# Kernel optimization log

Hardware: AMD Instinct MI355X
Metric: run time of the kernel (lower is better)

## Reference

```python
import jax, jax.numpy as jnp
import numpy as np

DIM = 2048
HEADS = 16
HEAD_DIM = DIM // HEADS


def setup_inputs() -> dict:
    key = jax.random.key(0)
    ks = jax.random.split(key, 9)
    B, S = 1, 4096
    X = jax.random.normal(ks[0], (B, S, DIM), dtype=jnp.float32)
    sc = 1.0 / np.sqrt(DIM)
    Wq = jax.random.normal(ks[1], (DIM, DIM), dtype=jnp.float32) * sc
    bq = jax.random.normal(ks[2], (DIM,), dtype=jnp.float32) * 0.01
    Wk = jax.random.normal(ks[3], (DIM, DIM), dtype=jnp.float32) * sc
    bk = jax.random.normal(ks[4], (DIM,), dtype=jnp.float32) * 0.01
    Wv = jax.random.normal(ks[5], (DIM, DIM), dtype=jnp.float32) * sc
    bv = jax.random.normal(ks[6], (DIM,), dtype=jnp.float32) * 0.01
    Wo = jax.random.normal(ks[7], (DIM, DIM), dtype=jnp.float32) * sc
    bo = jax.random.normal(ks[8], (DIM,), dtype=jnp.float32) * 0.01
    return {"X": X, "Wq": Wq, "bq": bq, "Wk": Wk, "bk": bk,
            "Wv": Wv, "bv": bv, "Wo": Wo, "bo": bo, "is_causal": 1}


def reference(X, Wq, bq, Wk, bk, Wv, bv, Wo, bo, is_causal):
    B, S, _ = X.shape
    # torch nn.Linear: y = x @ W^T + b
    Q = (X @ Wq.T + bq).reshape(B, S, HEADS, HEAD_DIM).transpose(0, 2, 1, 3)
    K = (X @ Wk.T + bk).reshape(B, S, HEADS, HEAD_DIM).transpose(0, 2, 1, 3)
    V = (X @ Wv.T + bv).reshape(B, S, HEADS, HEAD_DIM).transpose(0, 2, 1, 3)
    scores = jnp.einsum('bhqd,bhkd->bhqk', Q, K) / np.sqrt(HEAD_DIM)  # [B,H,S,S]
    if is_causal:
        causal = jnp.tril(jnp.ones((S, S), dtype=bool))
        scores = jnp.where(causal, scores, -jnp.inf)
    attn = jax.nn.softmax(scores, axis=-1)
    # dropout_rate = 0 (eval) -> identity
    Out = jnp.einsum('bhqk,bhkd->bhqd', attn, V)
    Out = Out.transpose(0, 2, 1, 3).reshape(B, S, DIM)
    return Out @ Wo.T + bo
```

## Files before the change

### kernel.cpp

```cpp
#include <hip/hip_runtime.h>
#include <hip/hip_bf16.h>

typedef unsigned short u16;
typedef __attribute__((ext_vector_type(8))) short short8;
typedef __attribute__((ext_vector_type(4))) short short4v;
typedef __attribute__((ext_vector_type(4))) float floatx4;

constexpr int SEQ = 4096;
constexpr int DM  = 2048;
constexpr int NH  = 16;
constexpr int HD  = 128;

__device__ inline u16 f2b(float f) {
    __hip_bfloat16 h = __float2bfloat16(f);
    return *reinterpret_cast<u16*>(&h);
}
__device__ inline float b2f(u16 u) {
    __hip_bfloat16 h = *reinterpret_cast<__hip_bfloat16*>(&u);
    return __bfloat162float(h);
}

__device__ __forceinline__ void async_copy16(const u16* g, u16* lds_base) {
    __builtin_amdgcn_global_load_lds(
        (const __attribute__((address_space(1))) unsigned int*)g,
        (__attribute__((address_space(3))) unsigned int*)lds_base,
        16, 0, 0);
}

__global__ void detect_dtype(const u16* __restrict__ X, int* __restrict__ flag) {
    __shared__ int cnt;
    if (threadIdx.x == 0) cnt = 0;
    __syncthreads();
    int local = 0;
    for (int i = threadIdx.x; i < 4096; i += 256) {
        int e = (X[i] >> 7) & 0xFF;
        if (e >= 0x3C && e <= 0x8D) local++;
    }
    atomicAdd(&cnt, local);
    __syncthreads();
    if (threadIdx.x == 0) *flag = (cnt >= 3890) ? 1 : 0;
}

struct ConvArgs {
    const void* src[9];
    unsigned long long dstoff[9];
    int n[9];
};
__global__ void convert_all(ConvArgs a, u16* __restrict__ base,
                            const int* __restrict__ flag) {
    const int t = blockIdx.y;
    const int n = a.n[t];
    const int i = (blockIdx.x * blockDim.x + threadIdx.x) * 8;
    if (i >= n) return;
    u16* out = base + a.dstoff[t];
    if (*flag) {
        *(short8*)&out[i] = *(const short8*)&((const u16*)a.src[t])[i];
    } else {
        const float* p = (const float*)a.src[t];
        u16 tmp[8];
#pragma unroll
        for (int j = 0; j < 8; j++) tmp[j] = f2b(p[i + j]);
        *(short8*)&out[i] = *(const short8*)tmp;
    }
}

__device__ __forceinline__ void gemm256_core(
    const u16* __restrict__ A, const u16* __restrict__ W,
    int m0, int n0, floatx4 (&acc)[8][4])
{
    __shared__ __align__(16) u16 As[2][16384];
    __shared__ __align__(16) u16 Bs[2][16384];
    constexpr int K  = DM;
    constexpr int NT = K / 64;

    const int tid  = threadIdx.x;
    const int lane = tid & 63;
    const int w    = tid >> 6;
    const int qm   = lane & 15;
    const int quad = lane >> 4;
    const int wm   = (w >> 2) * 128;
    const int wn   = (w & 3) * 64;

    const int srow = tid >> 3;
    const int scol = ((tid & 7) ^ (srow & 7)) * 8;

    const int fo0 = (quad ^ (qm & 7)) * 8;
    const int fo1 = fo0 ^ 32;

    const u16* Ag = A + (size_t)(m0 + srow) * K + scol;
    const u16* Wg = W + (size_t)(n0 + srow) * K + scol;

#define STG_A4(par, k0) {                                                 \
    async_copy16(Ag + (size_t)0 * 64 * K + (k0), &As[par][0 * 4096 + w * 512]); \
    async_copy16(Ag + (size_t)1 * 64 * K + (k0), &As[par][1 * 4096 + w * 512]); \
    async_copy16(Ag + (size_t)2 * 64 * K + (k0), &As[par][2 * 4096 + w * 512]); \
    async_copy16(Ag + (size_t)3 * 64 * K + (k0), &As[par][3 * 4096 + w * 512]); }
#define STG_B4(par, k0) {                                                 \
    async_copy16(Wg + (size_t)0 * 64 * K + (k0), &Bs[par][0 * 4096 + w * 512]); \
    async_copy16(Wg + (size_t)1 * 64 * K + (k0), &Bs[par][1 * 4096 + w * 512]); \
    async_copy16(Wg + (size_t)2 * 64 * K + (k0), &Bs[par][2 * 4096 + w * 512]); \
    async_copy16(Wg + (size_t)3 * 64 * K + (k0), &Bs[par][3 * 4096 + w * 512]); }

#define RD_A(d0, d1, row) { d0 = *(const short8*)&Ac[(row) * 64 + fo0];   \
                            d1 = *(const short8*)&Ac[(row) * 64 + fo1]; }

#define MFMA_Q(q2, x00, x01, x10, x11) {                                  \
    __builtin_amdgcn_s_setprio(1);                                        \
    _Pragma("unroll")                                                     \
    for (int nt = 0; nt < 4; ++nt) {                                      \
        acc[q2][nt]     = __builtin_amdgcn_mfma_f32_16x16x32_bf16(x00, bf[nt][0], acc[q2][nt], 0, 0, 0);     \
        acc[q2][nt]     = __builtin_amdgcn_mfma_f32_16x16x32_bf16(x01, bf[nt][1], acc[q2][nt], 0, 0, 0);     \
        acc[q2 + 1][nt] = __builtin_amdgcn_mfma_f32_16x16x32_bf16(x10, bf[nt][0], acc[q2 + 1][nt], 0, 0, 0); \
        acc[q2 + 1][nt] = __builtin_amdgcn_mfma_f32_16x16x32_bf16(x11, bf[nt][1], acc[q2 + 1][nt], 0, 0, 0); \
    }                                                                     \
    __builtin_amdgcn_s_setprio(0); }

#pragma unroll
    for (int i = 0; i < 8; ++i)
#pragma unroll
        for (int j = 0; j < 4; ++j) acc[i][j] = floatx4{0.f, 0.f, 0.f, 0.f};

    STG_A4(0, 0);
    STG_B4(0, 0);
    STG_A4(1, 64);
    STG_B4(1, 64);
    asm volatile("s_waitcnt vmcnt(8)" ::: "memory");
    __builtin_amdgcn_s_barrier();
    asm volatile("" ::: "memory");

    for (int t = 0; t < NT; ++t) {
        const int p = t & 1;
        const u16* Ac = As[p];
        const u16* Bc = Bs[p];
        const bool more = (t + 2 < NT);
        const int kf = (t + 2) * 64;

        short8 bf[4][2];
        short8 a0, a1, a2, a3, b0, b1, b2, b3;
        short8 c0, c1, c2, c3, d0, d1, d2, d3;

#pragma unroll
        for (int nt = 0; nt < 4; ++nt) {
            const int br = wn + nt * 16 + qm;
            bf[nt][0] = *(const short8*)&Bc[br * 64 + fo0];
            bf[nt][1] = *(const short8*)&Bc[br * 64 + fo1];
        }
        RD_A(a0, a1, wm + qm);
        RD_A(a2, a3, wm + 16 + qm);
        RD_A(b0, b1, wm + 32 + qm);
        RD_A(b2, b3, wm + 48 + qm);
        MFMA_Q(0, a0, a1, a2, a3);

        RD_A(c0, c1, wm + 64 + qm);
        RD_A(c2, c3, wm + 80 + qm);
        MFMA_Q(2, b0, b1, b2, b3);

        asm volatile("" ::: "memory");
        __builtin_amdgcn_s_barrier();
        asm volatile("" ::: "memory");
        if (more) { STG_B4(p, kf); }

        RD_A(d0, d1, wm + 96 + qm);
        RD_A(d2, d3, wm + 112 + qm);
        MFMA_Q(4, c0, c1, c2, c3);

        MFMA_Q(6, d0, d1, d2, d3);

        if (more) asm volatile("s_waitcnt vmcnt(4)" ::: "memory");
        else      asm volatile("s_waitcnt vmcnt(0)" ::: "memory");
        __builtin_amdgcn_s_barrier();
        asm volatile("" ::: "memory");
        if (more) { STG_A4(p, kf); }
    }
#undef STG_A4
#undef STG_B4
#undef RD_A
#undef MFMA_Q
}

__launch_bounds__(512, 2)
__global__ void gemm_qkv(const u16* __restrict__ A, const u16* __restrict__ W,
                         const u16* __restrict__ bias,
                         u16* __restrict__ Qb, u16* __restrict__ Kb,
                         u16* __restrict__ VtG) {
    const int m0 = blockIdx.y * 256;
    const int n0 = blockIdx.x * 256;
    floatx4 acc[8][4];
    gemm256_core(A, W, m0, n0, acc);

    const int tid  = threadIdx.x;
    const int lane = tid & 63;
    const int w    = tid >> 6;
    const int qm   = lane & 15;
    const int quad = lane >> 4;
    const int wm   = (w >> 2) * 128;
    const int wn   = (w & 3) * 64;

    const int buf = n0 >> 11;
    if (buf < 2) {
        u16* Y = (buf == 0) ? Qb : Kb;
#pragma unroll
        for (int nt = 0; nt < 4; ++nt) {
            const int gcol = n0 + wn + nt * 16 + qm;
            const int col  = gcol & 2047;
            const float bv = b2f(bias[gcol]);
#pragma unroll
            for (int mt = 0; mt < 8; ++mt) {
                const int rbase = m0 + wm + mt * 16 + quad * 4;
#pragma unroll
                for (int r = 0; r < 4; ++r)
                    Y[(size_t)(rbase + r) * DM + col] = f2b(acc[mt][nt][r] + bv);
            }
        }
    } else {
#pragma unroll
        for (int nt = 0; nt < 4; ++nt) {
            const int gcol = n0 + wn + nt * 16 + qm;
            const int col  = gcol & 2047;
            const float bv = b2f(bias[gcol]);
#pragma unroll
            for (int mt = 0; mt < 8; ++mt) {
                const int rbase = m0 + wm + mt * 16 + quad * 4;
                u16 tmp[4];
#pragma unroll
                for (int r = 0; r < 4; ++r)
                    tmp[r] = f2b(acc[mt][nt][r] + bv);
                *(short4v*)&VtG[(size_t)col * SEQ + rbase] = *(const short4v*)tmp;
            }
        }
    }
}

__launch_bounds__(512, 2)
__global__ void gemm_out(const u16* __restrict__ A, const u16* __restrict__ W,
                         const u16* __restrict__ bias, void* __restrict__ out,
                         const int* __restrict__ flag) {
    const int m0 = blockIdx.y * 256;
    const int n0 = blockIdx.x * 256;
    floatx4 acc[8][4];
    gemm256_core(A, W, m0, n0, acc);

    const int tid  = threadIdx.x;
    const int lane = tid & 63;
    const int w    = tid >> 6;
    const int qm   = lane & 15;
    const int quad = lane >> 4;
    const int wm   = (w >> 2) * 128;
    const int wn   = (w & 3) * 64;
    const int N    = DM;

    const int f = *flag;
#pragma unroll
    for (int nt = 0; nt < 4; ++nt) {
        const int col = n0 + wn + nt * 16 + qm;
        const float bv = b2f(bias[col]);
#pragma unroll
        for (int mt = 0; mt < 8; ++mt) {
            const int rbase = m0 + wm + mt * 16 + quad * 4;
#pragma unroll
            for (int r = 0; r < 4; ++r) {
                const float v = acc[mt][nt][r] + bv;
                if (f) ((u16*)out)[(size_t)(rbase + r) * N + col] = f2b(v);
                else   ((float*)out)[(size_t)(rbase + r) * N + col] = v;
            }
        }
    }
}

__launch_bounds__(512)
__global__ void attn_kernel(const u16* __restrict__ Q, const u16* __restrict__ K,
                            const u16* __restrict__ Vt, u16* __restrict__ O,
                            const int* __restrict__ is_causal_p) {
    __shared__ __align__(16) u16 Ks[64][136];
    __shared__ __align__(16) u16 Vts[128][72];
    __shared__ __align__(16) u16 Pb[8][16][72];

    const int tid  = threadIdx.x;
    const int lane = tid & 63;
    const int w    = tid >> 6;
    const int qm   = lane & 15;
    const int quad = lane >> 4;
    const int xt   = ((blockIdx.y >> 3) & 1) ? (gridDim.x - 1 - blockIdx.x)
                                             : blockIdx.x;
    const int q0   = xt * 128;
    const int h    = blockIdx.y;
    const int causal = *is_causal_p;
    const float scale = 0.08838834764831845f;
    const float SHIFT = 16.0f;

    short8 qf[4];
    {
        const u16* qptr = Q + (size_t)(q0 + w * 16 + qm) * DM + h * HD;
#pragma unroll
        for (int kc = 0; kc < 4; kc++)
            qf[kc] = *(const short8*)&qptr[kc * 32 + quad * 8];
    }

    floatx4 o[8];
#pragma unroll
    for (int dt = 0; dt < 8; dt++) o[dt] = floatx4{0.f, 0.f, 0.f, 0.f};
    float l_part[4] = {0.f, 0.f, 0.f, 0.f};

    const int jend = causal ? (q0 + 128) : SEQ;

    const int kr0 = tid >> 4;
    const int kc8 = (tid & 15) * 8;
    const int vd0 = tid >> 3;
    const int vc8 = (tid & 7) * 8;

    short8 kreg[2], vreg[2];
#pragma unroll
    for (int p = 0; p < 2; p++) {
        kreg[p] = *(const short8*)&K[(size_t)(kr0 + p * 32) * DM + h * HD + kc8];
        vreg[p] = *(const short8*)&Vt[(size_t)(h * HD + vd0 + p * 64) * SEQ + vc8];
    }

    for (int j0 = 0; j0 < jend; j0 += 64) {
#pragma unroll
        for (int p = 0; p < 2; p++) {
            *(short8*)&Ks[kr0 + p * 32][kc8] = kreg[p];
            *(short8*)&Vts[vd0 + p * 64][vc8] = vreg[p];
        }
        __syncthreads();

        const int jn = (j0 + 64 < jend) ? j0 + 64 : 0;
#pragma unroll
        for (int p = 0; p < 2; p++) {
            kreg[p] = *(const short8*)&K[(size_t)(jn + kr0 + p * 32) * DM + h * HD + kc8];
            vreg[p] = *(const short8*)&Vt[(size_t)(h * HD + vd0 + p * 64) * SEQ + jn + vc8];
        }

        floatx4 s[4];
#pragma unroll
        for (int nt = 0; nt < 4; nt++) s[nt] = floatx4{0.f, 0.f, 0.f, 0.f};
#pragma unroll
        for (int kc = 0; kc < 4; kc++)
#pragma unroll
            for (int nt = 0; nt < 4; nt++) {
                short8 b = *(const short8*)&Ks[nt * 16 + qm][kc * 32 + quad * 8];
                s[nt] = __builtin_amdgcn_mfma_f32_16x16x32_bf16(qf[kc], b, s[nt], 0, 0, 0);
            }

        const bool mask = causal && (j0 + 64 > q0 + w * 16);
#pragma unroll
        for (int r = 0; r < 4; r++) {
            const int qg = q0 + w * 16 + quad * 4 + r;
#pragma unroll
            for (int nt = 0; nt < 4; nt++) {
                float v = fmaf(s[nt][r], scale, -SHIFT);
                if (mask && (j0 + nt * 16 + qm > qg)) v = -1e30f;
                const float p = __expf(v);
                l_part[r] += p;
                Pb[w][quad * 4 + r][nt * 16 + qm] = f2b(p);
            }
        }
        asm volatile("s_waitcnt lgkmcnt(0)" ::: "memory");

#pragma unroll
        for (int kc = 0; kc < 2; kc++) {
            short8 pf = *(const short8*)&Pb[w][qm][kc * 32 + quad * 8];
#pragma unroll
            for (int dt = 0; dt < 8; dt++) {
                short8 b = *(const short8*)&Vts[dt * 16 + qm][kc * 32 + quad * 8];
                o[dt] = __builtin_amdgcn_mfma_f32_16x16x32_bf16(pf, b, o[dt], 0, 0, 0);
            }
        }
        __syncthreads();
    }

#pragma unroll
    for (int r = 0; r < 4; r++) {
        float l = l_part[r];
#pragma unroll
        for (int off = 8; off >= 1; off >>= 1)
            l += __shfl_xor(l, off, 64);
        const float inv = 1.0f / l;
        const int qg = q0 + w * 16 + quad * 4 + r;
#pragma unroll
        for (int dt = 0; dt < 8; dt++) {
            const int d = h * HD + dt * 16 + qm;
            O[(size_t)qg * DM + d] = f2b(o[dt][r] * inv);
        }
    }
}

extern "C" void kernel_launch(void* const* d_in, const int* in_sizes, int n_in,
                              void* d_out, int out_size, void* d_ws, size_t ws_size,
                              hipStream_t stream) {
    const int* isc = (const int*)d_in[9];

    int* flag = (int*)d_ws;
    u16* base = (u16*)((char*)d_ws + 256);

    const int NX = SEQ * DM;
    const int NW = DM * DM;
    const int NB = DM;

    unsigned long long off = 0;
    const unsigned long long oXc   = off; off += NX;
    const unsigned long long oWall = off; off += 3ull * NW;
    const unsigned long long oWo   = off; off += NW;
    const unsigned long long oBall = off; off += 3ull * NB;
    const unsigned long long oBo   = off; off += NB;
    const unsigned long long oQ    = off; off += NX;
    const unsigned long long oK    = off; off += NX;
    const unsigned long long oVt   = off; off += NX;
    const unsigned long long oA    = off; off += NX;

    detect_dtype<<<1, 256, 0, stream>>>((const u16*)d_in[0], flag);

    ConvArgs ca;
    const unsigned long long dsts[9] = {oXc, oWall, oBall, oWall + NW, oBall + NB,
                                        oWall + 2ull * NW, oBall + 2ull * NB, oWo, oBo};
    for (int i = 0; i < 9; i++) {
        ca.src[i] = d_in[i];
        ca.dstoff[i] = dsts[i];
        ca.n[i] = in_sizes[i];
    }
    convert_all<<<dim3(NX / 8 / 256, 9), 256, 0, stream>>>(ca, base, flag);

    gemm_qkv<<<dim3(3 * DM / 256, SEQ / 256), 512, 0, stream>>>(
        base + oXc, base + oWall, base + oBall,
        base + oQ, base + oK, base + oVt);

    attn_kernel<<<dim3(SEQ / 128, NH), 512, 0, stream>>>(
        base + oQ, base + oK, base + oVt, base + oA, isc);

    gemm_out<<<dim3(DM / 256, SEQ / 256), 512, 0, stream>>>(
        base + oA, base + oWo, base + oBo, d_out, flag);
}
```

Baseline: 479.7 us.

## Shrink GEMM tiles to 256x128 to raise block count

Replaces the 256x256 GEMM tile with a 256x128 tile in both the QKV and output projections. Each wave now covers 64x64 instead of 128x64, the B staging and wait counts are halved to match, and the grids double. The aim is to fill more of the CUs, since the output GEMM previously launched only 128 blocks, and to reduce register pressure. The cost is lower arithmetic intensity per block, with more A-tile reloads and less operand reuse per MFMA.

```diff
diff --git a/kernel.cpp b/kernel.cpp
--- a/kernel.cpp
+++ b/kernel.cpp
@@ -64,12 +64,12 @@
     }
 }
 
-__device__ __forceinline__ void gemm256_core(
+__device__ __forceinline__ void gemm256x128_core(
     const u16* __restrict__ A, const u16* __restrict__ W,
-    int m0, int n0, floatx4 (&acc)[8][4])
+    int m0, int n0, floatx4 (&acc)[4][4])
 {
     __shared__ __align__(16) u16 As[2][16384];
-    __shared__ __align__(16) u16 Bs[2][16384];
+    __shared__ __align__(16) u16 Bs[2][8192];
     constexpr int K  = DM;
     constexpr int NT = K / 64;
 
@@ -78,8 +78,8 @@
     const int w    = tid >> 6;
     const int qm   = lane & 15;
     const int quad = lane >> 4;
-    const int wm   = (w >> 2) * 128;
-    const int wn   = (w & 3) * 64;
+    const int wm   = (w >> 1) * 64;
+    const int wn   = (w & 1) * 64;
 
     const int srow = tid >> 3;
     const int scol = ((tid & 7) ^ (srow & 7)) * 8;
@@ -95,36 +95,32 @@
     async_copy16(Ag + (size_t)1 * 64 * K + (k0), &As[par][1 * 4096 + w * 512]); \
     async_copy16(Ag + (size_t)2 * 64 * K + (k0), &As[par][2 * 4096 + w * 512]); \
     async_copy16(Ag + (size_t)3 * 64 * K + (k0), &As[par][3 * 4096 + w * 512]); }
-#define STG_B4(par, k0) {                                                 \
+#define STG_B2(par, k0) {                                                 \
     async_copy16(Wg + (size_t)0 * 64 * K + (k0), &Bs[par][0 * 4096 + w * 512]); \
-    async_copy16(Wg + (size_t)1 * 64 * K + (k0), &Bs[par][1 * 4096 + w * 512]); \
-    async_copy16(Wg + (size_t)2 * 64 * K + (k0), &Bs[par][2 * 4096 + w * 512]); \
-    async_copy16(Wg + (size_t)3 * 64 * K + (k0), &Bs[par][3 * 4096 + w * 512]); }
+    async_copy16(Wg + (size_t)1 * 64 * K + (k0), &Bs[par][1 * 4096 + w * 512]); }
 
 #define RD_A(d0, d1, row) { d0 = *(const short8*)&Ac[(row) * 64 + fo0];   \
                             d1 = *(const short8*)&Ac[(row) * 64 + fo1]; }
 
-#define MFMA_Q(q2, x00, x01, x10, x11) {                                  \
+#define MFMA_G(g, x0, x1) {                                               \
     __builtin_amdgcn_s_setprio(1);                                        \
     _Pragma("unroll")                                                     \
     for (int nt = 0; nt < 4; ++nt) {                                      \
-        acc[q2][nt]     = __builtin_amdgcn_mfma_f32_16x16x32_bf16(x00, bf[nt][0], acc[q2][nt], 0, 0, 0);     \
-        acc[q2][nt]     = __builtin_amdgcn_mfma_f32_16x16x32_bf16(x01, bf[nt][1], acc[q2][nt], 0, 0, 0);     \
-        acc[q2 + 1][nt] = __builtin_amdgcn_mfma_f32_16x16x32_bf16(x10, bf[nt][0], acc[q2 + 1][nt], 0, 0, 0); \
-        acc[q2 + 1][nt] = __builtin_amdgcn_mfma_f32_16x16x32_bf16(x11, bf[nt][1], acc[q2 + 1][nt], 0, 0, 0); \
+        acc[g][nt] = __builtin_amdgcn_mfma_f32_16x16x32_bf16(x0, rB[nt][0], acc[g][nt], 0, 0, 0); \
+        acc[g][nt] = __builtin_amdgcn_mfma_f32_16x16x32_bf16(x1, rB[nt][1], acc[g][nt], 0, 0, 0); \
     }                                                                     \
     __builtin_amdgcn_s_setprio(0); }
 
 #pragma unroll
-    for (int i = 0; i < 8; ++i)
+    for (int i = 0; i < 4; ++i)
 #pragma unroll
         for (int j = 0; j < 4; ++j) acc[i][j] = floatx4{0.f, 0.f, 0.f, 0.f};
 
     STG_A4(0, 0);
-    STG_B4(0, 0);
+    STG_B2(0, 0);
     STG_A4(1, 64);
-    STG_B4(1, 64);
-    asm volatile("s_waitcnt vmcnt(8)" ::: "memory");
+    STG_B2(1, 64);
+    asm volatile("s_waitcnt vmcnt(6)" ::: "memory");
     __builtin_amdgcn_s_barrier();
     asm volatile("" ::: "memory");
 
@@ -135,47 +131,42 @@
         const bool more = (t + 2 < NT);
         const int kf = (t + 2) * 64;
 
-        short8 bf[4][2];
-        short8 a0, a1, a2, a3, b0, b1, b2, b3;
-        short8 c0, c1, c2, c3, d0, d1, d2, d3;
+        short8 rB[4][2];
+        short8 a0, a1, a2, a3, b0, b1, c0, c1;
 
 #pragma unroll
         for (int nt = 0; nt < 4; ++nt) {
             const int br = wn + nt * 16 + qm;
-            bf[nt][0] = *(const short8*)&Bc[br * 64 + fo0];
-            bf[nt][1] = *(const short8*)&Bc[br * 64 + fo1];
+            rB[nt][0] = *(const short8*)&Bc[br * 64 + fo0];
+            rB[nt][1] = *(const short8*)&Bc[br * 64 + fo1];
         }
         RD_A(a0, a1, wm + qm);
         RD_A(a2, a3, wm + 16 + qm);
+        MFMA_G(0, a0, a1);
+
         RD_A(b0, b1, wm + 32 + qm);
-        RD_A(b2, b3, wm + 48 + qm);
-        MFMA_Q(0, a0, a1, a2, a3);
-
-        RD_A(c0, c1, wm + 64 + qm);
-        RD_A(c2, c3, wm + 80 + qm);
-        MFMA_Q(2, b0, b1, b2, b3);
+        MFMA_G(1, a2, a3);
 
         asm volatile("" ::: "memory");
         __builtin_amdgcn_s_barrier();
         asm volatile("" ::: "memory");
-        if (more) { STG_B4(p, kf); }
-
-        RD_A(d0, d1, wm + 96 + qm);
-        RD_A(d2, d3, wm + 112 + qm);
-        MFMA_Q(4, c0, c1, c2, c3);
-
-        MFMA_Q(6, d0, d1, d2, d3);
-
-        if (more) asm volatile("s_waitcnt vmcnt(4)" ::: "memory");
+        if (more) { STG_B2(p, kf); }
+
+        RD_A(c0, c1, wm + 48 + qm);
+        MFMA_G(2, b0, b1);
+
+        MFMA_G(3, c0, c1);
+
+        if (more) asm volatile("s_waitcnt vmcnt(2)" ::: "memory");
         else      asm volatile("s_waitcnt vmcnt(0)" ::: "memory");
         __builtin_amdgcn_s_barrier();
         asm volatile("" ::: "memory");
         if (more) { STG_A4(p, kf); }
     }
 #undef STG_A4
-#undef STG_B4
+#undef STG_B2
 #undef RD_A
-#undef MFMA_Q
+#undef MFMA_G
 }
 
 __launch_bounds__(512, 2)
@@ -184,17 +175,17 @@
                          u16* __restrict__ Qb, u16* __restrict__ Kb,
                          u16* __restrict__ VtG) {
     const int m0 = blockIdx.y * 256;
-    const int n0 = blockIdx.x * 256;
-    floatx4 acc[8][4];
-    gemm256_core(A, W, m0, n0, acc);
+    const int n0 = blockIdx.x * 128;
+    floatx4 acc[4][4];
+    gemm256x128_core(A, W, m0, n0, acc);
 
     const int tid  = threadIdx.x;
     const int lane = tid & 63;
     const int w    = tid >> 6;
     const int qm   = lane & 15;
     const int quad = lane >> 4;
-    const int wm   = (w >> 2) * 128;
-    const int wn   = (w & 3) * 64;
+    const int wm   = (w >> 1) * 64;
+    const int wn   = (w & 1) * 64;
 
     const int buf = n0 >> 11;
     if (buf < 2) {
@@ -205,7 +196,7 @@
             const int col  = gcol & 2047;
             const float bv = b2f(bias[gcol]);
 #pragma unroll
-            for (int mt = 0; mt < 8; ++mt) {
+            for (int mt = 0; mt < 4; ++mt) {
                 const int rbase = m0 + wm + mt * 16 + quad * 4;
 #pragma unroll
                 for (int r = 0; r < 4; ++r)
@@ -219,7 +210,7 @@
             const int col  = gcol & 2047;
             const float bv = b2f(bias[gcol]);
 #pragma unroll
-            for (int mt = 0; mt < 8; ++mt) {
+            for (int mt = 0; mt < 4; ++mt) {
                 const int rbase = m0 + wm + mt * 16 + quad * 4;
                 u16 tmp[4];
 #pragma unroll
@@ -236,17 +227,17 @@
                          const u16* __restrict__ bias, void* __restrict__ out,
                          const int* __restrict__ flag) {
     const int m0 = blockIdx.y * 256;
-    const int n0 = blockIdx.x * 256;
-    floatx4 acc[8][4];
-    gemm256_core(A, W, m0, n0, acc);
+    const int n0 = blockIdx.x * 128;
+    floatx4 acc[4][4];
+    gemm256x128_core(A, W, m0, n0, acc);
 
     const int tid  = threadIdx.x;
     const int lane = tid & 63;
     const int w    = tid >> 6;
     const int qm   = lane & 15;
     const int quad = lane >> 4;
-    const int wm   = (w >> 2) * 128;
-    const int wn   = (w & 3) * 64;
+    const int wm   = (w >> 1) * 64;
+    const int wn   = (w & 1) * 64;
     const int N    = DM;
 
     const int f = *flag;
@@ -255,7 +246,7 @@
         const int col = n0 + wn + nt * 16 + qm;
         const float bv = b2f(bias[col]);
 #pragma unroll
-        for (int mt = 0; mt < 8; ++mt) {
+        for (int mt = 0; mt < 4; ++mt) {
             const int rbase = m0 + wm + mt * 16 + quad * 4;
 #pragma unroll
             for (int r = 0; r < 4; ++r) {
@@ -419,13 +410,13 @@
     }
     convert_all<<<dim3(NX / 8 / 256, 9), 256, 0, stream>>>(ca, base, flag);
 
-    gemm_qkv<<<dim3(3 * DM / 256, SEQ / 256), 512, 0, stream>>>(
+    gemm_qkv<<<dim3(3 * DM / 128, SEQ / 256), 512, 0, stream>>>(
         base + oXc, base + oWall, base + oBall,
         base + oQ, base + oK, base + oVt);
 
     attn_kernel<<<dim3(SEQ / 128, NH), 512, 0, stream>>>(
         base + oQ, base + oK, base + oVt, base + oA, isc);
 
-    gemm_out<<<dim3(DM / 256, SEQ / 256), 512, 0, stream>>>(
+    gemm_out<<<dim3(DM / 128, SEQ / 256), 512, 0, stream>>>(
         base + oA, base + oWo, base + oBo, d_out, flag);
 }
```

After: 462.5 us. 3.6% less time.

## Restructure GEMM main loop into 4-phase ping-pong schedule with register prefetch

Applied to the files above, without the earlier changes.

Rewrites the 256x256 GEMM core loop as a two-tile unrolled body split into four MFMA phases. Each phase interleaves LDS fragment reads, async global-to-LDS stages and barriers, and the next tile's B and first A fragments are prefetched into alternate register sets. The aim is to overlap LDS reads and global loads with MFMA work and to spread the staging across the tile. In exchange it adds more barriers per tile and raises register pressure, and the waitcnt/barrier ordering assumes NT is even.

```diff
diff --git a/kernel.cpp b/kernel.cpp
--- a/kernel.cpp
+++ b/kernel.cpp
@@ -90,92 +90,107 @@
     const u16* Ag = A + (size_t)(m0 + srow) * K + scol;
     const u16* Wg = W + (size_t)(n0 + srow) * K + scol;
 
-#define STG_A4(par, k0) {                                                 \
+#define STG_A_ALL(par, k0) {                                                    \
     async_copy16(Ag + (size_t)0 * 64 * K + (k0), &As[par][0 * 4096 + w * 512]); \
     async_copy16(Ag + (size_t)1 * 64 * K + (k0), &As[par][1 * 4096 + w * 512]); \
     async_copy16(Ag + (size_t)2 * 64 * K + (k0), &As[par][2 * 4096 + w * 512]); \
     async_copy16(Ag + (size_t)3 * 64 * K + (k0), &As[par][3 * 4096 + w * 512]); }
-#define STG_B4(par, k0) {                                                 \
-    async_copy16(Wg + (size_t)0 * 64 * K + (k0), &Bs[par][0 * 4096 + w * 512]); \
-    async_copy16(Wg + (size_t)1 * 64 * K + (k0), &Bs[par][1 * 4096 + w * 512]); \
-    async_copy16(Wg + (size_t)2 * 64 * K + (k0), &Bs[par][2 * 4096 + w * 512]); \
-    async_copy16(Wg + (size_t)3 * 64 * K + (k0), &Bs[par][3 * 4096 + w * 512]); }
-
-#define RD_A(d0, d1, row) { d0 = *(const short8*)&Ac[(row) * 64 + fo0];   \
-                            d1 = *(const short8*)&Ac[(row) * 64 + fo1]; }
-
-#define MFMA_Q(q2, x00, x01, x10, x11) {                                  \
-    __builtin_amdgcn_s_setprio(1);                                        \
-    _Pragma("unroll")                                                     \
-    for (int nt = 0; nt < 4; ++nt) {                                      \
-        acc[q2][nt]     = __builtin_amdgcn_mfma_f32_16x16x32_bf16(x00, bf[nt][0], acc[q2][nt], 0, 0, 0);     \
-        acc[q2][nt]     = __builtin_amdgcn_mfma_f32_16x16x32_bf16(x01, bf[nt][1], acc[q2][nt], 0, 0, 0);     \
-        acc[q2 + 1][nt] = __builtin_amdgcn_mfma_f32_16x16x32_bf16(x10, bf[nt][0], acc[q2 + 1][nt], 0, 0, 0); \
-        acc[q2 + 1][nt] = __builtin_amdgcn_mfma_f32_16x16x32_bf16(x11, bf[nt][1], acc[q2 + 1][nt], 0, 0, 0); \
-    }                                                                     \
+#define STG_B_H(h, par, k0) {                                                   \
+    async_copy16(Wg + (size_t)(2*(h)) * 64 * K + (k0),                          \
+                 &Bs[par][(2*(h)) * 4096 + w * 512]);                           \
+    async_copy16(Wg + (size_t)(2*(h)+1) * 64 * K + (k0),                        \
+                 &Bs[par][(2*(h)+1) * 4096 + w * 512]); }
+
+#define RD_AQ(dst, Abase, q) {                                                  \
+    dst[0][0] = *(const short8*)&Abase[(wm + (2*(q)) * 16 + qm) * 64 + fo0];    \
+    dst[0][1] = *(const short8*)&Abase[(wm + (2*(q)) * 16 + qm) * 64 + fo1];    \
+    dst[1][0] = *(const short8*)&Abase[(wm + (2*(q)+1) * 16 + qm) * 64 + fo0];  \
+    dst[1][1] = *(const short8*)&Abase[(wm + (2*(q)+1) * 16 + qm) * 64 + fo1]; }
+
+#define RD_B(dst, Bbase) {                                                      \
+    _Pragma("unroll")                                                           \
+    for (int nt = 0; nt < 4; ++nt) {                                            \
+        dst[nt][0] = *(const short8*)&Bbase[(wn + nt * 16 + qm) * 64 + fo0];    \
+        dst[nt][1] = *(const short8*)&Bbase[(wn + nt * 16 + qm) * 64 + fo1];    \
+    } }
+
+#define MFMA_Q(q, aR, bR) {                                                     \
+    __builtin_amdgcn_s_setprio(1);                                              \
+    _Pragma("unroll")                                                           \
+    for (int nt = 0; nt < 4; ++nt) {                                            \
+        acc[2*(q)][nt]   = __builtin_amdgcn_mfma_f32_16x16x32_bf16(aR[0][0], bR[nt][0], acc[2*(q)][nt],   0, 0, 0); \
+        acc[2*(q)][nt]   = __builtin_amdgcn_mfma_f32_16x16x32_bf16(aR[0][1], bR[nt][1], acc[2*(q)][nt],   0, 0, 0); \
+        acc[2*(q)+1][nt] = __builtin_amdgcn_mfma_f32_16x16x32_bf16(aR[1][0], bR[nt][0], acc[2*(q)+1][nt], 0, 0, 0); \
+        acc[2*(q)+1][nt] = __builtin_amdgcn_mfma_f32_16x16x32_bf16(aR[1][1], bR[nt][1], acc[2*(q)+1][nt], 0, 0, 0); \
+    }                                                                           \
     __builtin_amdgcn_s_setprio(0); }
 
+#define TILE_BODY(T, BCUR, BNXT) {                                              \
+    const int P = (T) & 1;                                                      \
+    const u16* Ac = As[P];                                                      \
+    const int kA = ((T) + 1) * 64, kB = ((T) + 2) * 64;                         \
+    const bool m1 = (T) + 1 < NT, m2 = (T) + 2 < NT;                            \
+                                     \
+    RD_AQ(aY, Ac, 1);                                                           \
+    if (m1) STG_A_ALL(P ^ 1, kA);                                               \
+    __builtin_amdgcn_s_barrier();                                               \
+    asm volatile("s_waitcnt lgkmcnt(4)" ::: "memory");                          \
+    __builtin_amdgcn_sched_barrier(0);                                          \
+    MFMA_Q(0, aX, BCUR);                                                        \
+    __builtin_amdgcn_s_barrier();                                               \
+                                  \
+    RD_AQ(aX, Ac, 2);                                                           \
+    if (m2) STG_B_H(0, P, kB);                                                  \
+    __builtin_amdgcn_s_barrier();                                               \
+    asm volatile("s_waitcnt lgkmcnt(4)" ::: "memory");                          \
+    __builtin_amdgcn_sched_barrier(0);                                          \
+    MFMA_Q(1, aY, BCUR);                                                        \
+    __builtin_amdgcn_s_barrier();                                               \
+                   \
+    RD_AQ(aY, Ac, 3);                                                           \
+    if (m2) STG_B_H(1, P, kB);                                                  \
+    __builtin_amdgcn_s_barrier();                                               \
+    asm volatile("s_waitcnt lgkmcnt(4)" ::: "memory");                          \
+    __builtin_amdgcn_sched_barrier(0);                                          \
+    MFMA_Q(2, aX, BCUR);                                                        \
+    if (m2) { asm volatile("s_waitcnt vmcnt(4)" ::: "memory"); }                \
+    else    { asm volatile("s_waitcnt vmcnt(0)" ::: "memory"); }                \
+    __builtin_amdgcn_s_barrier();                                               \
+              \
+    if (m1) { RD_B(BNXT, Bs[P ^ 1]); RD_AQ(aX, As[P ^ 1], 0); }                 \
+    __builtin_amdgcn_s_barrier();                                               \
+    if (m1) { asm volatile("s_waitcnt lgkmcnt(12)" ::: "memory"); }             \
+    else    { asm volatile("s_waitcnt lgkmcnt(0)"  ::: "memory"); }             \
+    __builtin_amdgcn_sched_barrier(0);                                          \
+    MFMA_Q(3, aY, BCUR);                                                        \
+    __builtin_amdgcn_s_barrier(); }
+
 #pragma unroll
     for (int i = 0; i < 8; ++i)
 #pragma unroll
         for (int j = 0; j < 4; ++j) acc[i][j] = floatx4{0.f, 0.f, 0.f, 0.f};
 
-    STG_A4(0, 0);
-    STG_B4(0, 0);
-    STG_A4(1, 64);
-    STG_B4(1, 64);
-    asm volatile("s_waitcnt vmcnt(8)" ::: "memory");
+    short8 Bu[4][2], Bv[4][2];
+    short8 aX[2][2], aY[2][2];
+
+    STG_B_H(0, 0, 0); STG_B_H(1, 0, 0);
+    STG_A_ALL(0, 0);
+    STG_B_H(0, 1, 64); STG_B_H(1, 1, 64);
+    asm volatile("s_waitcnt vmcnt(4)" ::: "memory");
     __builtin_amdgcn_s_barrier();
-    asm volatile("" ::: "memory");
-
-    for (int t = 0; t < NT; ++t) {
-        const int p = t & 1;
-        const u16* Ac = As[p];
-        const u16* Bc = Bs[p];
-        const bool more = (t + 2 < NT);
-        const int kf = (t + 2) * 64;
-
-        short8 bf[4][2];
-        short8 a0, a1, a2, a3, b0, b1, b2, b3;
-        short8 c0, c1, c2, c3, d0, d1, d2, d3;
-
-#pragma unroll
-        for (int nt = 0; nt < 4; ++nt) {
-            const int br = wn + nt * 16 + qm;
-            bf[nt][0] = *(const short8*)&Bc[br * 64 + fo0];
-            bf[nt][1] = *(const short8*)&Bc[br * 64 + fo1];
-        }
-        RD_A(a0, a1, wm + qm);
-        RD_A(a2, a3, wm + 16 + qm);
-        RD_A(b0, b1, wm + 32 + qm);
-        RD_A(b2, b3, wm + 48 + qm);
-        MFMA_Q(0, a0, a1, a2, a3);
-
-        RD_A(c0, c1, wm + 64 + qm);
-        RD_A(c2, c3, wm + 80 + qm);
-        MFMA_Q(2, b0, b1, b2, b3);
-
-        asm volatile("" ::: "memory");
-        __builtin_amdgcn_s_barrier();
-        asm volatile("" ::: "memory");
-        if (more) { STG_B4(p, kf); }
-
-        RD_A(d0, d1, wm + 96 + qm);
-        RD_A(d2, d3, wm + 112 + qm);
-        MFMA_Q(4, c0, c1, c2, c3);
-
-        MFMA_Q(6, d0, d1, d2, d3);
-
-        if (more) asm volatile("s_waitcnt vmcnt(4)" ::: "memory");
-        else      asm volatile("s_waitcnt vmcnt(0)" ::: "memory");
-        __builtin_amdgcn_s_barrier();
-        asm volatile("" ::: "memory");
-        if (more) { STG_A4(p, kf); }
-    }
-#undef STG_A4
-#undef STG_B4
-#undef RD_A
+    RD_B(Bu, Bs[0]);
+    RD_AQ(aX, As[0], 0);
+
+    for (int t2 = 0; t2 < NT; t2 += 2) {
+        TILE_BODY(t2,     Bu, Bv);
+        TILE_BODY(t2 + 1, Bv, Bu);
+    }
+#undef STG_A_ALL
+#undef STG_B_H
+#undef RD_AQ
+#undef RD_B
 #undef MFMA_Q
+#undef TILE_BODY
 }
 
 __launch_bounds__(512, 2)
```

Result: slower. 489.7 us (+2.1%).
